# Optimization experiments

Hardware: AMD Instinct MI355X
Metric: run time of the kernel (lower is better)

The kernel has to match this reference:

```python
import jax, jax.numpy as jnp
import numpy as np

B, S, T, K = 128, 4, 16, 36   # questions, answer slots (hardcoded 4), max tags/slot, num boxes
VD, QD, H = 256, 256, 256
NB = B * S * T                # total tag rows = leading dim of v, q


def setup_inputs() -> dict:
    key = jax.random.key(0)
    ks = jax.random.split(key, 8)
    tags_attention = jnp.ones((B, S, T), dtype=jnp.int32)  # all slots full -> sum == NB
    v = jax.random.normal(ks[0], (NB, K, VD), jnp.float32)
    q = jax.random.normal(ks[1], (NB, QD), jnp.float32)
    # binary box mask, first box always valid
    bm = (jax.random.uniform(ks[2], (B, K)) < 0.85).astype(jnp.float32)
    box_mask = bm.at[:, 0].set(1.0)
    Wv = jax.random.normal(ks[3], (H, VD), jnp.float32) / np.sqrt(VD).astype(np.float32)
    bv = jnp.zeros((H,), jnp.float32)
    Wq = jax.random.normal(ks[4], (H, QD), jnp.float32) / np.sqrt(QD).astype(np.float32)
    bq = jnp.zeros((H,), jnp.float32)
    Wl = jax.random.normal(ks[5], (1, H), jnp.float32) / np.sqrt(H).astype(np.float32)
    bl = jnp.zeros((1,), jnp.float32)
    return dict(v=v, q=q, box_mask=box_mask, tags_attention=tags_attention,
                Wv=Wv, bv=bv, Wq=Wq, bq=bq, Wl=Wl, bl=bl)


def reference(v, q, box_mask, tags_attention, Wv, bv, Wq, bq, Wl, bl):
    # FCNet projections (weight-normed Linear + ReLU; dropout inactive at eval)
    v_proj = jax.nn.relu(jnp.einsum('nkd,hd->nkh', v, Wv) + bv)          # [N,K,H]
    q_proj = jax.nn.relu(q @ Wq.T + bq)                                   # [N,H]
    joint = v_proj * q_proj[:, None, :]                                   # [N,K,H]
    logits = jnp.einsum('nkh,h->nk', joint, Wl[0]) + bl[0]                # [N,K]

    # pad_sequence: ragged rows -> [B,S,T,K] via per-slot offsets + masked gather
    Bq, Ss, Tt = tags_attention.shape
    lengths = tags_attention.sum(-1)                                      # [B,S]
    flat_len = lengths.reshape(-1)
    offsets = jnp.concatenate([jnp.zeros((1,), flat_len.dtype),
                               jnp.cumsum(flat_len)[:-1]]).reshape(Bq, Ss)
    t = jnp.arange(Tt)
    idx = offsets[:, :, None] + t                                         # [B,S,T]
    valid = t[None, None, :] < lengths[:, :, None]                        # [B,S,T]
    gathered = logits[jnp.clip(idx, 0, logits.shape[0] - 1)]              # [B,S,T,K]
    logits_batch = jnp.where(valid[..., None], gathered, 0.0)

    # masked_softmax (r2c style): softmax(x*mask)*mask, renormalized
    mask = box_mask[:, None, None, :]                                     # [B,1,1,K]
    w = jax.nn.softmax(logits_batch * mask, axis=-1) * mask
    w = w / (w.sum(-1, keepdims=True) + 1e-13)
    return w
```

## Files before the change

### kernel.cpp

```cpp
#include <hip/hip_runtime.h>
#include <hip/hip_bf16.h>
#include <stdint.h>

#define NBROWS 8192
#define KBOX   36
#define MROWS  (NBROWS * KBOX)

typedef __attribute__((ext_vector_type(8))) short bf16x8;
typedef __attribute__((ext_vector_type(4))) float f32x4;

__device__ __forceinline__ unsigned short f2bf(float f) {
  unsigned int u = __float_as_uint(f);
  return (unsigned short)((u + 0x7fffu + ((u >> 16) & 1u)) >> 16);
}

__device__ __forceinline__ unsigned int pk2(float x, float y) {
  __hip_bfloat16 hx = __float2bfloat16(x);
  __hip_bfloat16 hy = __float2bfloat16(y);
  unsigned short ux, uy;
  __builtin_memcpy(&ux, &hx, 2);
  __builtin_memcpy(&uy, &hy, 2);
  return (unsigned)ux | ((unsigned)uy << 16);
}

#define LGKM_BARRIER() do {                                   \
    asm volatile("s_waitcnt lgkmcnt(0)" ::: "memory");        \
    asm volatile("s_barrier" ::: "memory");                   \
  } while (0)

__global__ void cvt_kernel(const float* __restrict__ Wv, const float* __restrict__ Wq,
                           unsigned short* __restrict__ wvb, unsigned short* __restrict__ wqb) {
  int i = blockIdx.x * 256 + threadIdx.x;
  wvb[i] = f2bf(Wv[i]);
  wqb[i] = f2bf(Wq[i]);
}

template<int MODE>
__global__ __launch_bounds__(256, 2)
void gemm_kernel(const float* __restrict__ Amat,
                 const unsigned short* __restrict__ Wbf,
                 const float* __restrict__ bias,
                 const float* __restrict__ wl,
                 const float* __restrict__ g,
                 float* __restrict__ outp,
                 const float* __restrict__ blp)
{
  __shared__ unsigned short Asm[2][64 * 32];
  __shared__ unsigned short Bsm[2][256 * 32];
  __shared__ float bias_sm[256];
  __shared__ float aux_sm[4 * 256];
  __shared__ float partial[64 * 4];

  const int t    = threadIdx.x;
  const int lane = t & 63;
  const int wid  = t >> 6;
  const int r0   = blockIdx.x * 64;

  bias_sm[t] = bias[t];
  int n_base = 0;
  if (MODE == 0) {
    aux_sm[t] = wl[t];
  } else {
    n_base = r0 / KBOX;
    #pragma unroll
    for (int i = 0; i < 4; ++i) {
      int idx = t + i * 256;
      int n = n_base + (idx >> 8);
      if (n > NBROWS - 1) n = NBROWS - 1;
      aux_sm[idx] = g[(size_t)n * 256 + (idx & 255)];
    }
  }

  const int brow = t >> 2;
  const int bko  = t & 3;
  const int arow = t >> 2;
  const int ako  = t & 3;
  const float* asrc = Amat + (size_t)(r0 + arow) * 256 + ako * 8;
  const int adst_off = arow * 32 + (ako ^ ((arow >> 1) & 3)) * 8;

  f32x4 acc[4][4];
  #pragma unroll
  for (int a = 0; a < 4; ++a)
    #pragma unroll
    for (int b = 0; b < 4; ++b) acc[a][b] = (f32x4)0.f;

  float4 aregA[2], aregB[2];
  uint4  breg[4];

  #pragma unroll
  for (int i = 0; i < 4; ++i)
    breg[i] = *(const uint4*)&Wbf[(brow + i * 64) * 256 + 0 + bko * 8];
  aregA[0] = ((const float4*)(asrc + 0))[0];
  aregA[1] = ((const float4*)(asrc + 0))[1];
  aregB[0] = ((const float4*)(asrc + 32))[0];
  aregB[1] = ((const float4*)(asrc + 32))[1];
  #pragma unroll
  for (int i = 0; i < 4; ++i) {
    int r = brow + i * 64;
    *(uint4*)&Bsm[0][r * 32 + (bko ^ ((r >> 1) & 3)) * 8] = breg[i];
  }
  {
    uint4 pk;
    pk.x = pk2(aregA[0].x, aregA[0].y);
    pk.y = pk2(aregA[0].z, aregA[0].w);
    pk.z = pk2(aregA[1].x, aregA[1].y);
    pk.w = pk2(aregA[1].z, aregA[1].w);
    *(uint4*)&Asm[0][adst_off] = pk;
  }
  LGKM_BARRIER();

  #pragma unroll
  for (int kk = 0; kk < 8; ++kk) {
    const int cur = kk & 1;
    if (kk < 7) {
      const int d0 = (kk + 1) * 32;
      #pragma unroll
      for (int i = 0; i < 4; ++i)
        breg[i] = *(const uint4*)&Wbf[(brow + i * 64) * 256 + d0 + bko * 8];
    }
    if (kk < 6) {
      const int d0 = (kk + 2) * 32;
      float4 t0 = ((const float4*)(asrc + d0))[0];
      float4 t1 = ((const float4*)(asrc + d0))[1];
      if (kk & 1) { aregB[0] = t0; aregB[1] = t1; }
      else        { aregA[0] = t0; aregA[1] = t1; }
    }
    bf16x8 af[4], bfr[4];
    #pragma unroll
    for (int mf = 0; mf < 4; ++mf) {
      int row  = mf * 16 + (lane & 15);
      int phys = (lane >> 4) ^ ((row >> 1) & 3);
      af[mf] = *(const bf16x8*)&Asm[cur][row * 32 + phys * 8];
    }
    #pragma unroll
    for (int nf = 0; nf < 4; ++nf) {
      int col  = wid * 64 + nf * 16 + (lane & 15);
      int phys = (lane >> 4) ^ ((col >> 1) & 3);
      bfr[nf] = *(const bf16x8*)&Bsm[cur][col * 32 + phys * 8];
    }
    #pragma unroll
    for (int mf = 0; mf < 4; ++mf)
      #pragma unroll
      for (int nf = 0; nf < 4; ++nf)
        acc[mf][nf] = __builtin_amdgcn_mfma_f32_16x16x32_bf16(af[mf], bfr[nf], acc[mf][nf], 0, 0, 0);
    if (kk < 7) {
      #pragma unroll
      for (int i = 0; i < 4; ++i) {
        int r = brow + i * 64;
        *(uint4*)&Bsm[1 - cur][r * 32 + (bko ^ ((r >> 1) & 3)) * 8] = breg[i];
      }
      const float4 a0 = (kk & 1) ? aregA[0] : aregB[0];
      const float4 a1 = (kk & 1) ? aregA[1] : aregB[1];
      uint4 pk;
      pk.x = pk2(a0.x, a0.y);
      pk.y = pk2(a0.z, a0.w);
      pk.z = pk2(a1.x, a1.y);
      pk.w = pk2(a1.z, a1.w);
      *(uint4*)&Asm[1 - cur][adst_off] = pk;
      LGKM_BARRIER();
    }
  }

  if (MODE == 0) {
    #pragma unroll
    for (int mf = 0; mf < 4; ++mf)
      #pragma unroll
      for (int nf = 0; nf < 4; ++nf) {
        int col = wid * 64 + nf * 16 + (lane & 15);
        float bb = bias_sm[col];
        float ww = aux_sm[col];
        #pragma unroll
        for (int j = 0; j < 4; ++j) {
          int row = mf * 16 + ((lane >> 4) << 2) + j;
          float x = fmaxf(acc[mf][nf][j] + bb, 0.f) * ww;
          outp[(size_t)(r0 + row) * 256 + col] = x;
        }
      }
  } else {
    float s[4][4];
    #pragma unroll
    for (int mf = 0; mf < 4; ++mf) {
      #pragma unroll
      for (int j = 0; j < 4; ++j) {
        int row  = mf * 16 + ((lane >> 4) << 2) + j;
        int nloc = (r0 + row) / KBOX - n_base;
        const float* grow = &aux_sm[nloc * 256];
        float acc_s = 0.f;
        #pragma unroll
        for (int nf = 0; nf < 4; ++nf) {
          int col = wid * 64 + nf * 16 + (lane & 15);
          float x = acc[mf][nf][j] + bias_sm[col];
          acc_s += fmaxf(x, 0.f) * grow[col];
        }
        s[mf][j] = acc_s;
      }
    }
    #pragma unroll
    for (int mf = 0; mf < 4; ++mf)
      #pragma unroll
      for (int j = 0; j < 4; ++j) {
        float vv = s[mf][j];
        vv += __shfl_xor(vv, 1);
        vv += __shfl_xor(vv, 2);
        vv += __shfl_xor(vv, 4);
        vv += __shfl_xor(vv, 8);
        s[mf][j] = vv;
      }
    if ((lane & 15) == 0) {
      #pragma unroll
      for (int mf = 0; mf < 4; ++mf)
        #pragma unroll
        for (int j = 0; j < 4; ++j) {
          int row = mf * 16 + ((lane >> 4) << 2) + j;
          partial[row * 4 + wid] = s[mf][j];
        }
    }
    __syncthreads();
    if (t < 64) {
      float vv = partial[t * 4 + 0] + partial[t * 4 + 1] + partial[t * 4 + 2] + partial[t * 4 + 3];
      outp[r0 + t] = vv + blp[0];
    }
  }
}

__global__ __launch_bounds__(256)
void softmax_kernel(const float* __restrict__ logits, const float* __restrict__ box_mask,
                    float* __restrict__ outp) {
  int n = blockIdx.x * 4 + (threadIdx.x >> 6);
  int k = threadIdx.x & 63;
  int b = n >> 6;
  float l = 0.f, m = 0.f;
  if (k < KBOX) {
    m = box_mask[b * KBOX + k];
    l = logits[(size_t)n * KBOX + k];
  }
  bool act = (k < KBOX) && (m > 0.5f);
  float lm = act ? l : -3.0e38f;
  #pragma unroll
  for (int off = 32; off >= 1; off >>= 1) lm = fmaxf(lm, __shfl_xor(lm, off));
  float e = act ? expf(l - lm) : 0.f;
  float ssum = e;
  #pragma unroll
  for (int off = 32; off >= 1; off >>= 1) ssum += __shfl_xor(ssum, off);
  if (k < KBOX) outp[(size_t)n * KBOX + k] = e / ssum;
}

extern "C" void kernel_launch(void* const* d_in, const int* in_sizes, int n_in,
                              void* d_out, int out_size, void* d_ws, size_t ws_size,
                              hipStream_t stream) {
  const float* v        = (const float*)d_in[0];
  const float* q        = (const float*)d_in[1];
  const float* box_mask = (const float*)d_in[2];
  const float* Wv = (const float*)d_in[4];
  const float* bv = (const float*)d_in[5];
  const float* Wq = (const float*)d_in[6];
  const float* bq = (const float*)d_in[7];
  const float* Wl = (const float*)d_in[8];
  const float* bl = (const float*)d_in[9];
  float* outp = (float*)d_out;

  char* ws = (char*)d_ws;
  unsigned short* wvb = (unsigned short*)ws;
  unsigned short* wqb = (unsigned short*)(ws + 131072);
  float* g      = (float*)(ws + 262144);
  float* logits = (float*)(ws + 262144 + 8388608);

  cvt_kernel<<<256, 256, 0, stream>>>(Wv, Wq, wvb, wqb);
  gemm_kernel<0><<<NBROWS / 64, 256, 0, stream>>>(q, wqb, bq, Wl, nullptr, g, nullptr);
  gemm_kernel<1><<<MROWS / 64, 256, 0, stream>>>(v, wvb, bv, nullptr, g, logits, bl);
  softmax_kernel<<<NBROWS / 4, 256, 0, stream>>>(logits, box_mask, outp);
}
```

Before: 116.1 us.

## Fuse v-projection GEMM with softmax in persistent weight-resident blocks

Replaces the per-64-row v GEMM and separate softmax kernel with a persistent kernel: 256 blocks of 512 threads, each processing 1152 rows (32 tag rows) in nine 128-row tiles. The full bf16 Wv matrix is loaded into LDS once per block instead of being streamed every k-step. Logits stay in shared memory and the masked softmax runs at the end of the same kernel, which removes the logits round-trip and one launch. The cost is a 128 KB LDS footprint, which allows only one block per CU, and only 256 blocks, which risks reduced occupancy and underused CUs.

```diff
diff --git a/kernel.cpp b/kernel.cpp
--- a/kernel.cpp
+++ b/kernel.cpp
@@ -5,6 +5,8 @@
 #define NBROWS 8192
 #define KBOX   36
 #define MROWS  (NBROWS * KBOX)
+#define RPB    1152
+#define NTILE  9
 
 typedef __attribute__((ext_vector_type(8))) short bf16x8;
 typedef __attribute__((ext_vector_type(4))) float f32x4;
@@ -35,21 +37,17 @@
   wqb[i] = f2bf(Wq[i]);
 }
 
-template<int MODE>
 __global__ __launch_bounds__(256, 2)
-void gemm_kernel(const float* __restrict__ Amat,
-                 const unsigned short* __restrict__ Wbf,
-                 const float* __restrict__ bias,
-                 const float* __restrict__ wl,
-                 const float* __restrict__ g,
-                 float* __restrict__ outp,
-                 const float* __restrict__ blp)
+void qproj_kernel(const float* __restrict__ Amat,
+                  const unsigned short* __restrict__ Wbf,
+                  const float* __restrict__ bias,
+                  const float* __restrict__ wl,
+                  float* __restrict__ outp)
 {
   __shared__ unsigned short Asm[2][64 * 32];
   __shared__ unsigned short Bsm[2][256 * 32];
   __shared__ float bias_sm[256];
-  __shared__ float aux_sm[4 * 256];
-  __shared__ float partial[64 * 4];
+  __shared__ float aux_sm[256];
 
   const int t    = threadIdx.x;
   const int lane = t & 63;
@@ -57,19 +55,7 @@
   const int r0   = blockIdx.x * 64;
 
   bias_sm[t] = bias[t];
-  int n_base = 0;
-  if (MODE == 0) {
-    aux_sm[t] = wl[t];
-  } else {
-    n_base = r0 / KBOX;
-    #pragma unroll
-    for (int i = 0; i < 4; ++i) {
-      int idx = t + i * 256;
-      int n = n_base + (idx >> 8);
-      if (n > NBROWS - 1) n = NBROWS - 1;
-      aux_sm[idx] = g[(size_t)n * 256 + (idx & 255)];
-    }
-  }
+  aux_sm[t]  = wl[t];
 
   const int brow = t >> 2;
   const int bko  = t & 3;
@@ -161,88 +147,206 @@
     }
   }
 
-  if (MODE == 0) {
-    #pragma unroll
-    for (int mf = 0; mf < 4; ++mf)
+  #pragma unroll
+  for (int mf = 0; mf < 4; ++mf)
+    #pragma unroll
+    for (int nf = 0; nf < 4; ++nf) {
+      int col = wid * 64 + nf * 16 + (lane & 15);
+      float bb = bias_sm[col];
+      float ww = aux_sm[col];
+      #pragma unroll
+      for (int j = 0; j < 4; ++j) {
+        int row = mf * 16 + ((lane >> 4) << 2) + j;
+        float x = fmaxf(acc[mf][nf][j] + bb, 0.f) * ww;
+        outp[(size_t)(r0 + row) * 256 + col] = x;
+      }
+    }
+}
+
+__global__ __launch_bounds__(512, 2)
+void vmain_kernel(const float* __restrict__ v,
+                  const unsigned short* __restrict__ Wbf,
+                  const float* __restrict__ bv,
+                  const float* __restrict__ g,
+                  const float* __restrict__ blp,
+                  const float* __restrict__ bmask,
+                  float* __restrict__ outp)
+{
+  __shared__ unsigned short Wlds[256 * 256];
+  __shared__ unsigned short Asm[2][128 * 32];
+  __shared__ float gtile[5 * 256];
+  __shared__ float partial[128 * 4];
+  __shared__ float logit_sm[RPB];
+
+  const int t    = threadIdx.x;
+  const int lane = t & 63;
+  const int wid  = t >> 6;
+  const int wn   = wid & 3;
+  const int wm   = wid >> 2;
+  const int l15  = lane & 15;
+  const int lq   = lane >> 4;
+  const int blk  = blockIdx.x;
+  const long long rowbase = (long long)blk * RPB;
+
+  #pragma unroll
+  for (int p = 0; p < 16; ++p) {
+    int flat = p * 512 + t;
+    int col  = flat >> 5;
+    int chk  = flat & 31;
+    uint4 w = *(const uint4*)&Wbf[col * 256 + chk * 8];
+    *(uint4*)&Wlds[col * 256 + (chk ^ (col & 7)) * 8] = w;
+  }
+
+  float bias_r[4];
+  #pragma unroll
+  for (int nf = 0; nf < 4; ++nf) bias_r[nf] = bv[wn * 64 + nf * 16 + l15];
+  const float blv = blp[0];
+
+  const int arow = t >> 2;
+  const int ako  = t & 3;
+  const float* asrc = v + (rowbase + arow) * 256 + ako * 8;
+  const int adst = arow * 32 + (ako ^ ((arow >> 1) & 3)) * 8;
+
+  float4 pA0[2], pA1[2];
+
+  pA0[0] = ((const float4*)(asrc + 0))[0];
+  pA0[1] = ((const float4*)(asrc + 0))[1];
+  pA1[0] = ((const float4*)(asrc + 32))[0];
+  pA1[1] = ((const float4*)(asrc + 32))[1];
+  {
+    uint4 pk;
+    pk.x = pk2(pA0[0].x, pA0[0].y);
+    pk.y = pk2(pA0[0].z, pA0[0].w);
+    pk.z = pk2(pA0[1].x, pA0[1].y);
+    pk.w = pk2(pA0[1].z, pA0[1].w);
+    *(uint4*)&Asm[0][adst] = pk;
+  }
+  LGKM_BARRIER();
+
+  f32x4 acc[4][4];
+  float gr[3];
+
+  #pragma unroll 1
+  for (int tile = 0; tile < NTILE; ++tile) {
+    #pragma unroll
+    for (int a = 0; a < 4; ++a)
+      #pragma unroll
+      for (int b = 0; b < 4; ++b) acc[a][b] = (f32x4)0.f;
+
+    const int m0  = (int)rowbase + tile * 128;
+    const int n0t = m0 / KBOX;
+
+    #pragma unroll
+    for (int kk = 0; kk < 8; ++kk) {
+      const int cur = kk & 1;
+      {
+        const float* p = nullptr;
+        if (kk < 6)                  p = asrc + tile * 32768 + (kk + 2) * 32;
+        else if (tile < NTILE - 1)   p = asrc + (tile + 1) * 32768 + (kk - 6) * 32;
+        if (p) {
+          float4 t0 = ((const float4*)p)[0];
+          float4 t1 = ((const float4*)p)[1];
+          if (kk & 1) { pA1[0] = t0; pA1[1] = t1; }
+          else        { pA0[0] = t0; pA0[1] = t1; }
+        }
+      }
+      if (kk == 0) {
+        #pragma unroll
+        for (int i = 0; i < 3; ++i) {
+          int idx = i * 512 + t;
+          if (idx < 1280) {
+            int n = n0t + (idx >> 8);
+            if (n > NBROWS - 1) n = NBROWS - 1;
+            gr[i] = g[(size_t)n * 256 + (idx & 255)];
+          }
+        }
+      }
+      bf16x8 af[4], bfr[4];
+      #pragma unroll
+      for (int mf = 0; mf < 4; ++mf) {
+        int row  = wm * 64 + mf * 16 + l15;
+        int phys = lq ^ ((row >> 1) & 3);
+        af[mf] = *(const bf16x8*)&Asm[cur][row * 32 + phys * 8];
+      }
       #pragma unroll
       for (int nf = 0; nf < 4; ++nf) {
-        int col = wid * 64 + nf * 16 + (lane & 15);
-        float bb = bias_sm[col];
-        float ww = aux_sm[col];
-        #pragma unroll
-        for (int j = 0; j < 4; ++j) {
-          int row = mf * 16 + ((lane >> 4) << 2) + j;
-          float x = fmaxf(acc[mf][nf][j] + bb, 0.f) * ww;
-          outp[(size_t)(r0 + row) * 256 + col] = x;
-        }
-      }
-  } else {
-    float s[4][4];
-    #pragma unroll
-    for (int mf = 0; mf < 4; ++mf) {
-      #pragma unroll
-      for (int j = 0; j < 4; ++j) {
-        int row  = mf * 16 + ((lane >> 4) << 2) + j;
-        int nloc = (r0 + row) / KBOX - n_base;
-        const float* grow = &aux_sm[nloc * 256];
-        float acc_s = 0.f;
-        #pragma unroll
-        for (int nf = 0; nf < 4; ++nf) {
-          int col = wid * 64 + nf * 16 + (lane & 15);
-          float x = acc[mf][nf][j] + bias_sm[col];
-          acc_s += fmaxf(x, 0.f) * grow[col];
-        }
-        s[mf][j] = acc_s;
-      }
-    }
-    #pragma unroll
-    for (int mf = 0; mf < 4; ++mf)
-      #pragma unroll
-      for (int j = 0; j < 4; ++j) {
-        float vv = s[mf][j];
-        vv += __shfl_xor(vv, 1);
-        vv += __shfl_xor(vv, 2);
-        vv += __shfl_xor(vv, 4);
-        vv += __shfl_xor(vv, 8);
-        s[mf][j] = vv;
-      }
-    if ((lane & 15) == 0) {
+        int col  = wn * 64 + nf * 16 + l15;
+        int phys = (kk * 4 + lq) ^ (col & 7);
+        bfr[nf] = *(const bf16x8*)&Wlds[col * 256 + phys * 8];
+      }
       #pragma unroll
       for (int mf = 0; mf < 4; ++mf)
         #pragma unroll
-        for (int j = 0; j < 4; ++j) {
-          int row = mf * 16 + ((lane >> 4) << 2) + j;
-          partial[row * 4 + wid] = s[mf][j];
+        for (int nf = 0; nf < 4; ++nf)
+          acc[mf][nf] = __builtin_amdgcn_mfma_f32_16x16x32_bf16(af[mf], bfr[nf], acc[mf][nf], 0, 0, 0);
+      if (kk < 7 || tile < NTILE - 1) {
+        const float4 a0 = (kk & 1) ? pA0[0] : pA1[0];
+        const float4 a1 = (kk & 1) ? pA0[1] : pA1[1];
+        uint4 pk;
+        pk.x = pk2(a0.x, a0.y);
+        pk.y = pk2(a0.z, a0.w);
+        pk.z = pk2(a1.x, a1.y);
+        pk.w = pk2(a1.z, a1.w);
+        *(uint4*)&Asm[1 - cur][adst] = pk;
+      }
+      if (kk == 1) {
+        #pragma unroll
+        for (int i = 0; i < 3; ++i) {
+          int idx = i * 512 + t;
+          if (idx < 1280) gtile[idx] = gr[i];
         }
-    }
-    __syncthreads();
-    if (t < 64) {
-      float vv = partial[t * 4 + 0] + partial[t * 4 + 1] + partial[t * 4 + 2] + partial[t * 4 + 3];
-      outp[r0 + t] = vv + blp[0];
-    }
-  }
-}
-
-__global__ __launch_bounds__(256)
-void softmax_kernel(const float* __restrict__ logits, const float* __restrict__ box_mask,
-                    float* __restrict__ outp) {
-  int n = blockIdx.x * 4 + (threadIdx.x >> 6);
-  int k = threadIdx.x & 63;
-  int b = n >> 6;
-  float l = 0.f, m = 0.f;
-  if (k < KBOX) {
-    m = box_mask[b * KBOX + k];
-    l = logits[(size_t)n * KBOX + k];
-  }
-  bool act = (k < KBOX) && (m > 0.5f);
-  float lm = act ? l : -3.0e38f;
-  #pragma unroll
-  for (int off = 32; off >= 1; off >>= 1) lm = fmaxf(lm, __shfl_xor(lm, off));
-  float e = act ? expf(l - lm) : 0.f;
-  float ssum = e;
-  #pragma unroll
-  for (int off = 32; off >= 1; off >>= 1) ssum += __shfl_xor(ssum, off);
-  if (k < KBOX) outp[(size_t)n * KBOX + k] = e / ssum;
+      }
+      if (kk == 7) {
+        #pragma unroll
+        for (int mf = 0; mf < 4; ++mf)
+          #pragma unroll
+          for (int j = 0; j < 4; ++j) {
+            int rloc = wm * 64 + mf * 16 + lq * 4 + j;
+            int nloc = (m0 + rloc) / KBOX - n0t;
+            const float* grow = &gtile[nloc * 256];
+            float sv = 0.f;
+            #pragma unroll
+            for (int nf = 0; nf < 4; ++nf) {
+              int col = wn * 64 + nf * 16 + l15;
+              sv += fmaxf(acc[mf][nf][j] + bias_r[nf], 0.f) * grow[col];
+            }
+            sv += __shfl_xor(sv, 1);
+            sv += __shfl_xor(sv, 2);
+            sv += __shfl_xor(sv, 4);
+            sv += __shfl_xor(sv, 8);
+            if (l15 == 0) partial[rloc * 4 + wn] = sv;
+          }
+      }
+      LGKM_BARRIER();
+      if (kk == 7 && t < 128) {
+        logit_sm[tile * 128 + t] = partial[t * 4 + 0] + partial[t * 4 + 1]
+                                 + partial[t * 4 + 2] + partial[t * 4 + 3] + blv;
+      }
+    }
+  }
+
+  LGKM_BARRIER();
+
+  const int batch = blk >> 1;
+  #pragma unroll
+  for (int i = 0; i < 4; ++i) {
+    int bx = wid * 4 + i;
+    long long bg = (long long)blk * 32 + bx;
+    float mk = 0.f, lv = 0.f;
+    if (lane < KBOX) {
+      mk = bmask[batch * KBOX + lane];
+      lv = logit_sm[bx * KBOX + lane];
+    }
+    bool act = (lane < KBOX) && (mk > 0.5f);
+    float lm = act ? lv : -3.0e38f;
+    #pragma unroll
+    for (int off = 32; off >= 1; off >>= 1) lm = fmaxf(lm, __shfl_xor(lm, off));
+    float e = act ? expf(lv - lm) : 0.f;
+    float ssum = e;
+    #pragma unroll
+    for (int off = 32; off >= 1; off >>= 1) ssum += __shfl_xor(ssum, off);
+    if (lane < KBOX) outp[bg * KBOX + lane] = e / ssum;
+  }
 }
 
 extern "C" void kernel_launch(void* const* d_in, const int* in_sizes, int n_in,
@@ -262,11 +366,9 @@
   char* ws = (char*)d_ws;
   unsigned short* wvb = (unsigned short*)ws;
   unsigned short* wqb = (unsigned short*)(ws + 131072);
-  float* g      = (float*)(ws + 262144);
-  float* logits = (float*)(ws + 262144 + 8388608);
+  float* g = (float*)(ws + 262144);
 
   cvt_kernel<<<256, 256, 0, stream>>>(Wv, Wq, wvb, wqb);
-  gemm_kernel<0><<<NBROWS / 64, 256, 0, stream>>>(q, wqb, bq, Wl, nullptr, g, nullptr);
-  gemm_kernel<1><<<MROWS / 64, 256, 0, stream>>>(v, wvb, bv, nullptr, g, logits, bl);
-  softmax_kernel<<<NBROWS / 4, 256, 0, stream>>>(logits, box_mask, outp);
-}
+  qproj_kernel<<<NBROWS / 64, 256, 0, stream>>>(q, wqb, bq, Wl, g);
+  vmain_kernel<<<256, 512, 0, stream>>>(v, wvb, bv, g, bl, box_mask, outp);
+}
```

Result: no change. 114.4 us (-1.5%).

## Split v-GEMM into 512-thread kernel loading whole A tile upfront

Applied to the files above, without the earlier changes.

The large v projection GEMM moves into its own kernel with 512 threads arranged as 2x4 waves. It loads and converts the entire 64x256 fp32 A tile to bf16 in LDS at the start, instead of double-buffering 32-wide K slices. Only the small weight slices are still streamed, two steps ahead. The aim is to issue all A global loads at once for more memory-level parallelism and to cut per-step A conversion work, at the cost of more LDS per block and fewer accumulators per wave.

```diff
diff --git a/kernel.cpp b/kernel.cpp
--- a/kernel.cpp
+++ b/kernel.cpp
@@ -35,21 +35,17 @@
   wqb[i] = f2bf(Wq[i]);
 }
 
-template<int MODE>
 __global__ __launch_bounds__(256, 2)
-void gemm_kernel(const float* __restrict__ Amat,
-                 const unsigned short* __restrict__ Wbf,
-                 const float* __restrict__ bias,
-                 const float* __restrict__ wl,
-                 const float* __restrict__ g,
-                 float* __restrict__ outp,
-                 const float* __restrict__ blp)
+void qproj_kernel(const float* __restrict__ Amat,
+                  const unsigned short* __restrict__ Wbf,
+                  const float* __restrict__ bias,
+                  const float* __restrict__ wl,
+                  float* __restrict__ outp)
 {
   __shared__ unsigned short Asm[2][64 * 32];
   __shared__ unsigned short Bsm[2][256 * 32];
   __shared__ float bias_sm[256];
-  __shared__ float aux_sm[4 * 256];
-  __shared__ float partial[64 * 4];
+  __shared__ float aux_sm[256];
 
   const int t    = threadIdx.x;
   const int lane = t & 63;
@@ -57,19 +53,7 @@
   const int r0   = blockIdx.x * 64;
 
   bias_sm[t] = bias[t];
-  int n_base = 0;
-  if (MODE == 0) {
-    aux_sm[t] = wl[t];
-  } else {
-    n_base = r0 / KBOX;
-    #pragma unroll
-    for (int i = 0; i < 4; ++i) {
-      int idx = t + i * 256;
-      int n = n_base + (idx >> 8);
-      if (n > NBROWS - 1) n = NBROWS - 1;
-      aux_sm[idx] = g[(size_t)n * 256 + (idx & 255)];
-    }
-  }
+  aux_sm[t]  = wl[t];
 
   const int brow = t >> 2;
   const int bko  = t & 3;
@@ -161,65 +145,155 @@
     }
   }
 
-  if (MODE == 0) {
-    #pragma unroll
-    for (int mf = 0; mf < 4; ++mf)
+  #pragma unroll
+  for (int mf = 0; mf < 4; ++mf)
+    #pragma unroll
+    for (int nf = 0; nf < 4; ++nf) {
+      int col = wid * 64 + nf * 16 + (lane & 15);
+      float bb = bias_sm[col];
+      float ww = aux_sm[col];
+      #pragma unroll
+      for (int j = 0; j < 4; ++j) {
+        int row = mf * 16 + ((lane >> 4) << 2) + j;
+        float x = fmaxf(acc[mf][nf][j] + bb, 0.f) * ww;
+        outp[(size_t)(r0 + row) * 256 + col] = x;
+      }
+    }
+}
+
+__global__ __launch_bounds__(512, 4)
+void vmain_kernel(const float* __restrict__ v,
+                  const unsigned short* __restrict__ wvb,
+                  const float* __restrict__ bv,
+                  const float* __restrict__ g,
+                  const float* __restrict__ blp,
+                  float* __restrict__ outp)
+{
+  __shared__ unsigned short Asm[64 * 256];
+  __shared__ unsigned short Bsm[2][256 * 32];
+  __shared__ float bias_sm[256];
+  __shared__ float gtile[4 * 256];
+  __shared__ float partial[64 * 4];
+
+  const int t    = threadIdx.x;
+  const int lane = t & 63;
+  const int wid  = t >> 6;
+  const int wn   = wid & 3;
+  const int wm   = wid >> 2;
+  const int l15  = lane & 15;
+  const int lq   = lane >> 4;
+  const int r0   = blockIdx.x * 64;
+  const int n0   = r0 / KBOX;
+
+  if (t < 256) bias_sm[t] = bv[t];
+  {
+    int idx = t;
+    int n = n0 + (idx >> 8);
+    if (n > NBROWS - 1) n = NBROWS - 1;
+    gtile[idx] = g[(size_t)n * 256 + (idx & 255)];
+    idx = t + 512;
+    n = n0 + (idx >> 8);
+    if (n > NBROWS - 1) n = NBROWS - 1;
+    gtile[idx] = g[(size_t)n * 256 + (idx & 255)];
+  }
+
+  const int bh0 = t >> 2;
+  const int bko = t & 3;
+  const int bd0 = bh0 * 32 + ((bko ^ ((bh0 >> 1) & 3)) << 3);
+  const int bh1 = bh0 + 128;
+  const int bd1 = bh1 * 32 + ((bko ^ ((bh1 >> 1) & 3)) << 3);
+
+  uint4 brg[2][2];
+  #define BISS(j) do {                                                            \
+      brg[(j) & 1][0] = *(const uint4*)&wvb[(size_t)bh0 * 256 + (j) * 32 + bko * 8]; \
+      brg[(j) & 1][1] = *(const uint4*)&wvb[(size_t)bh1 * 256 + (j) * 32 + bko * 8]; \
+    } while (0)
+  #define BWRT(j) do {                                                            \
+      *(uint4*)&Bsm[(j) & 1][bd0] = brg[(j) & 1][0];                              \
+      *(uint4*)&Bsm[(j) & 1][bd1] = brg[(j) & 1][1];                              \
+    } while (0)
+
+  {
+    BISS(0);
+    BISS(1);
+    const float* base = v + (size_t)(r0 + wid * 8) * 256 + lane * 4;
+    float4 ld[8];
+    #pragma unroll
+    for (int i = 0; i < 8; ++i) ld[i] = *(const float4*)(base + i * 256);
+    #pragma unroll
+    for (int i = 0; i < 8; ++i) {
+      int row = wid * 8 + i;
+      uint2 w_;
+      w_.x = pk2(ld[i].x, ld[i].y);
+      w_.y = pk2(ld[i].z, ld[i].w);
+      *(uint2*)&Asm[row * 256 + (((lane >> 1) ^ (row & 7)) << 3) + ((lane & 1) << 2)] = w_;
+    }
+    BWRT(0);
+  }
+  __syncthreads();
+
+  f32x4 acc[2][4];
+  #pragma unroll
+  for (int a = 0; a < 2; ++a)
+    #pragma unroll
+    for (int b = 0; b < 4; ++b) acc[a][b] = (f32x4)0.f;
+
+  #define STEP(kk)                                                                \
+  do {                                                                            \
+    if ((kk) < 6) BISS((kk) + 2);                                                 \
+    bf16x8 af[2], bfr[4];                                                         \
+    _Pragma("unroll")                                                             \
+    for (int mf = 0; mf < 2; ++mf) {                                              \
+      int row  = wm * 32 + mf * 16 + l15;                                         \
+      int phys = ((kk) * 4 + lq) ^ (row & 7);                                     \
+      af[mf] = *(const bf16x8*)&Asm[row * 256 + phys * 8];                        \
+    }                                                                             \
+    _Pragma("unroll")                                                             \
+    for (int nf = 0; nf < 4; ++nf) {                                              \
+      int col  = wn * 64 + nf * 16 + l15;                                         \
+      int phys = lq ^ ((col >> 1) & 3);                                           \
+      bfr[nf] = *(const bf16x8*)&Bsm[(kk) & 1][col * 32 + phys * 8];              \
+    }                                                                             \
+    _Pragma("unroll")                                                             \
+    for (int mf = 0; mf < 2; ++mf)                                                \
+      _Pragma("unroll")                                                           \
+      for (int nf = 0; nf < 4; ++nf)                                              \
+        acc[mf][nf] = __builtin_amdgcn_mfma_f32_16x16x32_bf16(af[mf], bfr[nf], acc[mf][nf], 0, 0, 0); \
+    if ((kk) < 7) {                                                               \
+      BWRT((kk) + 1);     \
+      LGKM_BARRIER();                                                             \
+    }                                                                             \
+  } while (0)
+
+  STEP(0); STEP(1); STEP(2); STEP(3);
+  STEP(4); STEP(5); STEP(6); STEP(7);
+  #undef STEP
+  #undef BISS
+  #undef BWRT
+
+  #pragma unroll
+  for (int mf = 0; mf < 2; ++mf)
+    #pragma unroll
+    for (int j = 0; j < 4; ++j) {
+      int rloc = wm * 32 + mf * 16 + lq * 4 + j;
+      int nl   = (r0 + rloc) / KBOX - n0;
+      const float* grow = &gtile[nl * 256];
+      float sv = 0.f;
       #pragma unroll
       for (int nf = 0; nf < 4; ++nf) {
-        int col = wid * 64 + nf * 16 + (lane & 15);
-        float bb = bias_sm[col];
-        float ww = aux_sm[col];
-        #pragma unroll
-        for (int j = 0; j < 4; ++j) {
-          int row = mf * 16 + ((lane >> 4) << 2) + j;
-          float x = fmaxf(acc[mf][nf][j] + bb, 0.f) * ww;
-          outp[(size_t)(r0 + row) * 256 + col] = x;
-        }
+        int col = wn * 64 + nf * 16 + l15;
+        sv += fmaxf(acc[mf][nf][j] + bias_sm[col], 0.f) * grow[col];
       }
-  } else {
-    float s[4][4];
-    #pragma unroll
-    for (int mf = 0; mf < 4; ++mf) {
-      #pragma unroll
-      for (int j = 0; j < 4; ++j) {
-        int row  = mf * 16 + ((lane >> 4) << 2) + j;
-        int nloc = (r0 + row) / KBOX - n_base;
-        const float* grow = &aux_sm[nloc * 256];
-        float acc_s = 0.f;
-        #pragma unroll
-        for (int nf = 0; nf < 4; ++nf) {
-          int col = wid * 64 + nf * 16 + (lane & 15);
-          float x = acc[mf][nf][j] + bias_sm[col];
-          acc_s += fmaxf(x, 0.f) * grow[col];
-        }
-        s[mf][j] = acc_s;
-      }
-    }
-    #pragma unroll
-    for (int mf = 0; mf < 4; ++mf)
-      #pragma unroll
-      for (int j = 0; j < 4; ++j) {
-        float vv = s[mf][j];
-        vv += __shfl_xor(vv, 1);
-        vv += __shfl_xor(vv, 2);
-        vv += __shfl_xor(vv, 4);
-        vv += __shfl_xor(vv, 8);
-        s[mf][j] = vv;
-      }
-    if ((lane & 15) == 0) {
-      #pragma unroll
-      for (int mf = 0; mf < 4; ++mf)
-        #pragma unroll
-        for (int j = 0; j < 4; ++j) {
-          int row = mf * 16 + ((lane >> 4) << 2) + j;
-          partial[row * 4 + wid] = s[mf][j];
-        }
-    }
-    __syncthreads();
-    if (t < 64) {
-      float vv = partial[t * 4 + 0] + partial[t * 4 + 1] + partial[t * 4 + 2] + partial[t * 4 + 3];
-      outp[r0 + t] = vv + blp[0];
-    }
+      sv += __shfl_xor(sv, 1);
+      sv += __shfl_xor(sv, 2);
+      sv += __shfl_xor(sv, 4);
+      sv += __shfl_xor(sv, 8);
+      if (l15 == 0) partial[rloc * 4 + wn] = sv;
+    }
+  __syncthreads();
+  if (t < 64) {
+    outp[r0 + t] = partial[t * 4 + 0] + partial[t * 4 + 1]
+                 + partial[t * 4 + 2] + partial[t * 4 + 3] + blp[0];
   }
 }
 
@@ -266,7 +340,7 @@
   float* logits = (float*)(ws + 262144 + 8388608);
 
   cvt_kernel<<<256, 256, 0, stream>>>(Wv, Wq, wvb, wqb);
-  gemm_kernel<0><<<NBROWS / 64, 256, 0, stream>>>(q, wqb, bq, Wl, nullptr, g, nullptr);
-  gemm_kernel<1><<<MROWS / 64, 256, 0, stream>>>(v, wvb, bv, nullptr, g, logits, bl);
+  qproj_kernel<<<NBROWS / 64, 256, 0, stream>>>(q, wqb, bq, Wl, g);
+  vmain_kernel<<<MROWS / 64, 512, 0, stream>>>(v, wvb, bv, g, bl, logits);
   softmax_kernel<<<NBROWS / 4, 256, 0, stream>>>(logits, box_mask, outp);
 }
```

New measurement: 164.1 us. 41.4% more time.
